# Performance work log

Hardware: AMD Instinct MI355X
Metric: run time of the kernel (lower is better)

The kernel has to match this reference:

```python
import jax, jax.numpy as jnp
import numpy as np

N_LORAS = 8   # number of adapters (experts)
RANK = 16     # rank per adapter; rmoe = N_LORAS * RANK = 128
TEMP = 1.0    # self.T


def setup_inputs() -> dict:
    key = jax.random.key(0)
    ks = jax.random.split(key, 7)
    B, S, D_IN, D_OUT = 4, 2048, 4096, 4096
    RMOE = N_LORAS * RANK
    x = jax.random.normal(ks[0], (B, S, D_IN), dtype=jnp.float32)
    base_w = jax.random.normal(ks[1], (D_OUT, D_IN), dtype=jnp.float32) / np.sqrt(D_IN)
    base_b = jax.random.normal(ks[2], (D_OUT,), dtype=jnp.float32) * 0.01
    # nn.init.normal_(lora_A.weight, std=1/r); lora_B zero-init in torch, use small random here
    lora_A = jax.random.normal(ks[3], (RMOE, D_IN), dtype=jnp.float32) / RANK
    lora_B = jax.random.normal(ks[4], (D_OUT, RMOE), dtype=jnp.float32) * 0.02
    router_w = jax.random.normal(ks[5], (N_LORAS, D_IN), dtype=jnp.float32) / np.sqrt(D_IN)
    # scaling[name] = lora_alpha / sqrt(r) per adapter (use_rslora)
    scalings = jnp.full((N_LORAS,), 32.0 / np.sqrt(RANK), dtype=jnp.float32)
    return {"x": x, "base_w": base_w, "base_b": base_b, "lora_A": lora_A,
            "lora_B": lora_B, "router_w": router_w, "scalings": scalings, "top_k": 2}


def reference(x, base_w, base_b, lora_A, lora_B, router_w, scalings, top_k):
    # Base dense layer: y = x W^T + b
    base_out = jnp.einsum('bsd,od->bso', x, base_w) + base_b

    # Router: per-token logits over adapters, top-k, softmax over selected
    logits = jnp.einsum('bsd,ed->bse', x, router_w) / TEMP          # [B,S,E]
    topv, topi = jax.lax.top_k(logits, top_k)                        # [B,S,K]
    gate_k = jax.nn.softmax(topv, axis=-1)                           # [B,S,K]
    # dense per-expert gate: scatter top-k weights back to E slots
    gate_e = jnp.sum(jax.nn.one_hot(topi, N_LORAS, dtype=gate_k.dtype)
                     * gate_k[..., None], axis=-2)                   # [B,S,E]

    # Fused LoRA: h = x A^T over the concatenated rank dim, mask ranks by gate*scaling
    h = jnp.einsum('bsd,rd->bsr', x, lora_A)                         # [B,S,RMOE]
    rank_w = jnp.repeat(gate_e * scalings, RANK, axis=-1)            # [B,S,RMOE]
    lora_out = jnp.einsum('bsr,or->bso', h * rank_w, lora_B)         # [B,S,O]

    return base_out + lora_out
```

## Files before the change

### kernel.cpp

```cpp
#include <hip/hip_runtime.h>
#include <cstdint>

typedef unsigned short u16;
typedef float  f32x4 __attribute__((ext_vector_type(4)));
typedef short  s16x4 __attribute__((ext_vector_type(4)));
typedef short  s16x8 __attribute__((ext_vector_type(8)));

#define D_IN  4096
#define D_OUT 4096
#define RMOE  128
#define KAUG  4224
#define NTOK  8192

__device__ __forceinline__ u16 f2bf(float f) {
    unsigned u = __builtin_bit_cast(unsigned, f);
    unsigned r = u + 0x7fffu + ((u >> 16) & 1u);
    return (u16)(r >> 16);
}

__device__ __forceinline__ void gload16(const void* g, void* l) {
    __builtin_amdgcn_global_load_lds(
        (const __attribute__((address_space(1))) void*)g,
        (__attribute__((address_space(3))) void*)l, 16, 0, 0);
}

__global__ __launch_bounds__(256)
void prep_kernel(const float* __restrict__ x, const float* __restrict__ rw,
                 const float* __restrict__ scal, const float* __restrict__ bw,
                 const float* __restrict__ lA, const float* __restrict__ lB,
                 u16* __restrict__ Xaug, u16* __restrict__ Waug,
                 u16* __restrict__ A16, float* __restrict__ gates) {
    if (blockIdx.x < 2048) {
        int wave = threadIdx.x >> 6, lane = threadIdx.x & 63;
        int t = blockIdx.x * 4 + wave;
        const float4* xp = (const float4*)(x + (long)t * D_IN);
        u16* xa = Xaug + (long)t * KAUG;
        float acc[8];
#pragma unroll
        for (int e = 0; e < 8; ++e) acc[e] = 0.f;
#pragma unroll 4
        for (int i = 0; i < 16; ++i) {
            float4 xv = xp[i * 64 + lane];
            s16x4 o;
            o[0] = (short)f2bf(xv.x); o[1] = (short)f2bf(xv.y);
            o[2] = (short)f2bf(xv.z); o[3] = (short)f2bf(xv.w);
            *(s16x4*)(xa + (i * 64 + lane) * 4) = o;
#pragma unroll
            for (int e = 0; e < 8; ++e) {
                float4 wv = ((const float4*)(rw + (long)e * D_IN))[i * 64 + lane];
                acc[e] += xv.x * wv.x + xv.y * wv.y + xv.z * wv.z + xv.w * wv.w;
            }
        }
#pragma unroll
        for (int e = 0; e < 8; ++e) {
#pragma unroll
            for (int off = 32; off > 0; off >>= 1)
                acc[e] += __shfl_xor(acc[e], off, 64);
        }
        if (lane == 0) {
            int i1 = 0; float v1 = acc[0];
#pragma unroll
            for (int e = 1; e < 8; ++e) if (acc[e] > v1) { v1 = acc[e]; i1 = e; }
            int i2 = -1; float v2 = -3.4e38f;
#pragma unroll
            for (int e = 0; e < 8; ++e) if (e != i1 && acc[e] > v2) { v2 = acc[e]; i2 = e; }
            float g1 = 1.f / (1.f + expf(v2 - v1));
            float g2 = 1.f - g1;
            float* gp = gates + (long)t * 8;
#pragma unroll
            for (int e = 0; e < 8; ++e)
                gp[e] = (e == i1) ? g1 * scal[e] : ((e == i2) ? g2 * scal[e] : 0.f);
        }
    } else {
        const long nw = (long)D_OUT * D_IN / 8;
        const long nb = (long)D_OUT * RMOE / 8;
        long tid = (long)(blockIdx.x - 2048) * 256 + threadIdx.x;
        const float* src; u16* dst;
        if (tid < nw) {
            long e = tid * 8; long row = e >> 12; long col = e & 4095;
            src = bw + e; dst = Waug + row * KAUG + col;
        } else if (tid < nw + nb) {
            long e = (tid - nw) * 8; long row = e >> 7; long col = e & 127;
            src = lB + e; dst = Waug + row * KAUG + D_IN + col;
        } else {
            long e = (tid - nw - nb) * 8;
            src = lA + e; dst = A16 + e;
        }
        float4 a = ((const float4*)src)[0];
        float4 b = ((const float4*)src)[1];
        s16x8 o;
        o[0] = (short)f2bf(a.x); o[1] = (short)f2bf(a.y);
        o[2] = (short)f2bf(a.z); o[3] = (short)f2bf(a.w);
        o[4] = (short)f2bf(b.x); o[5] = (short)f2bf(b.y);
        o[6] = (short)f2bf(b.z); o[7] = (short)f2bf(b.w);
        *(s16x8*)dst = o;
    }
}

__global__ __launch_bounds__(256)
void lora_h_kernel(u16* __restrict__ Xaug, const u16* __restrict__ A16,
                   const float* __restrict__ gates) {
    __shared__ u16 sX[64 * 32];
    __shared__ u16 sW[32 * 32];
    int tid = threadIdx.x, wave = tid >> 6, lane = tid & 63;
    int bm = blockIdx.x >> 2, bn = blockIdx.x & 3;
    long m0 = (long)bm * 64; int n0 = bn * 32;
    int wr = wave >> 1, wc = wave & 1;
    int rowA = tid >> 2, oct = tid & 3;
    const u16* gx = Xaug + (m0 + rowA) * KAUG + oct * 8;
    const u16* gw = A16 + (long)(n0 + rowA) * D_IN + oct * 8;
    u16* lx = sX + wave * 512;
    u16* lw = sW + wave * 512;
    int cl = lane & 15, kh = lane >> 4;
    int aoff[2];
#pragma unroll
    for (int i = 0; i < 2; ++i)
        aoff[i] = (wr * 32 + i * 16 + cl) * 32 + kh * 8;
    int boff = (wc * 16 + cl) * 32 + kh * 8;
    f32x4 acc2[2];
    acc2[0] = (f32x4){0.f, 0.f, 0.f, 0.f};
    acc2[1] = (f32x4){0.f, 0.f, 0.f, 0.f};
    for (int kt = 0; kt < 128; ++kt) {
        __syncthreads();
        gload16(gx, lx);
        if (tid < 128) gload16(gw, lw);
        gx += 32; gw += 32;
        __syncthreads();
        s16x8 a[2], b;
        a[0] = *(const s16x8*)&sX[aoff[0]];
        a[1] = *(const s16x8*)&sX[aoff[1]];
        b = *(const s16x8*)&sW[boff];
#pragma unroll
        for (int mi = 0; mi < 2; ++mi)
            acc2[mi] = __builtin_amdgcn_mfma_f32_16x16x32_bf16(
                a[mi], b, acc2[mi], 0, 0, 0);
    }
    int col = n0 + wc * 16 + cl;
    int g = col >> 4;
#pragma unroll
    for (int mi = 0; mi < 2; ++mi) {
#pragma unroll
        for (int r = 0; r < 4; ++r) {
            long tok = m0 + wr * 32 + mi * 16 + kh * 4 + r;
            float v = acc2[mi][r] * gates[tok * 8 + g];
            Xaug[tok * KAUG + D_IN + col] = f2bf(v);
        }
    }
}

__global__ __launch_bounds__(512, 4)
void main_gemm(const u16* __restrict__ Xaug, const u16* __restrict__ Waug,
               const float* __restrict__ bias, float* __restrict__ out) {
    __shared__ u16 lds[2 * 12288];
    const int tid = threadIdx.x;
    const int wave = tid >> 6, lane = tid & 63;
    const int cl = lane & 15, kh = lane >> 4;
    const int wr = wave >> 1, wc = wave & 1;

    int bid = blockIdx.x;
    int swz = (bid & 7) * 128 + (bid >> 3);
    long m0 = (long)(swz & 31) * 256;
    long n0 = (long)(swz >> 5) * 128;

    const int rA = tid >> 2;
    const int sl = (((tid & 3) ^ ((tid >> 3) & 3))) * 8;
    const u16* gA0 = Xaug + (m0 + rA) * KAUG + sl;
    const u16* gA1 = Xaug + (m0 + 128 + rA) * KAUG + sl;
    const u16* gB0 = Waug + (n0 + rA) * KAUG + sl;
    const int wbase = wave * 512;

    const int swk = (kh ^ ((cl >> 1) & 3)) * 8;
    const int aob = (wr * 64 + cl) * 32 + swk;
    const int bob = 8192 + (wc * 64 + cl) * 32 + swk;

    f32x4 acc[4][4];
#pragma unroll
    for (int m = 0; m < 4; ++m)
#pragma unroll
        for (int n = 0; n < 4; ++n) acc[m][n] = (f32x4){0.f, 0.f, 0.f, 0.f};

#define STAGE(t) do { u16* L = lds + ((t) & 1) * 12288 + wbase;              \
        gload16(gA0 + (t) * 32, L);                                          \
        gload16(gA1 + (t) * 32, L + 4096);                                   \
        gload16(gB0 + (t) * 32, L + 8192); } while (0)

    s16x8 av[4], bv[4];

    STAGE(0);

    for (int t = 0; t < 132; ++t) {
        asm volatile("s_waitcnt vmcnt(0)" ::: "memory");
        __builtin_amdgcn_s_barrier();
        __builtin_amdgcn_sched_barrier(0);
        if (t + 1 < 132) STAGE(t + 1);
        const u16* Lb = lds + (t & 1) * 12288;
#pragma unroll
        for (int m = 0; m < 4; ++m) av[m] = *(const s16x8*)&Lb[aob + m * 512];
#pragma unroll
        for (int n = 0; n < 4; ++n) bv[n] = *(const s16x8*)&Lb[bob + n * 512];
        asm volatile("s_waitcnt lgkmcnt(0)" ::: "memory");
        __builtin_amdgcn_sched_barrier(0);
        __builtin_amdgcn_s_setprio(1);
#pragma unroll
        for (int m = 0; m < 4; ++m)
#pragma unroll
            for (int n = 0; n < 4; ++n)
                acc[m][n] = __builtin_amdgcn_mfma_f32_16x16x32_bf16(
                    av[m], bv[n], acc[m][n], 0, 0, 0);
        __builtin_amdgcn_s_setprio(0);
    }
#undef STAGE

#pragma unroll
    for (int n = 0; n < 4; ++n) {
        long col = n0 + wc * 64 + n * 16 + cl;
        float bvv = bias[col];
#pragma unroll
        for (int m = 0; m < 4; ++m) {
            long row = m0 + wr * 64 + m * 16 + kh * 4;
#pragma unroll
            for (int r = 0; r < 4; ++r)
                out[(row + r) * (long)D_OUT + col] = acc[m][n][r] + bvv;
        }
    }
}

extern "C" void kernel_launch(void* const* d_in, const int* in_sizes, int n_in,
                              void* d_out, int out_size, void* d_ws, size_t ws_size,
                              hipStream_t stream) {
    const float* x  = (const float*)d_in[0];
    const float* bw = (const float*)d_in[1];
    const float* bb = (const float*)d_in[2];
    const float* lA = (const float*)d_in[3];
    const float* lB = (const float*)d_in[4];
    const float* rw = (const float*)d_in[5];
    const float* sc = (const float*)d_in[6];
    float* out = (float*)d_out;

    char* ws = (char*)d_ws;
    u16* Xaug  = (u16*)ws;
    u16* Waug  = (u16*)(ws + 69206016);
    u16* A16   = (u16*)(ws + 103809024);
    float* gates = (float*)(ws + 104857600);

    prep_kernel<<<10752, 256, 0, stream>>>(x, rw, sc, bw, lA, lB,
                                           Xaug, Waug, A16, gates);
    lora_h_kernel<<<512, 256, 0, stream>>>(Xaug, A16, gates);
    main_gemm<<<1024, 512, 0, stream>>>(Xaug, Waug, bb, out);
}
```

Baseline: 418.4 us.

## Enlarge main GEMM tile to 256x256 with K=64 stages and interleaved MFMA/loads

Grows the main GEMM block tile from 256x128 to 256x256, so each of the 8 waves now computes a 128x64 output patch. The K step per stage goes from 32 to 64 with an 8-way XOR swizzle, and the grid is halved. The main loop is restructured into quarter-steps that interleave LDS reads, MFMA groups and async global-to-LDS loads, with partial vmcnt waits so prefetch overlaps compute. This raises arithmetic intensity and cuts global traffic per FLOP. In exchange it uses more LDS (128KB) and registers, lowers occupancy to 2 blocks per CU, and adds many more barriers per K step.

After: 380.1 us. 1.1x faster.

```diff
diff --git a/kernel.cpp b/kernel.cpp
--- a/kernel.cpp
+++ b/kernel.cpp
@@ -148,76 +148,123 @@
     }
 }
 
-__global__ __launch_bounds__(512, 4)
+__global__ __launch_bounds__(512, 2)
 void main_gemm(const u16* __restrict__ Xaug, const u16* __restrict__ Waug,
                const float* __restrict__ bias, float* __restrict__ out) {
-    __shared__ u16 lds[2 * 12288];
+    __shared__ u16 lds[65536];
     const int tid = threadIdx.x;
     const int wave = tid >> 6, lane = tid & 63;
     const int cl = lane & 15, kh = lane >> 4;
-    const int wr = wave >> 1, wc = wave & 1;
+    const int wr = wave >> 2, wc = wave & 3;
 
     int bid = blockIdx.x;
-    int swz = (bid & 7) * 128 + (bid >> 3);
+    int swz = (bid & 7) * 64 + (bid >> 3);
     long m0 = (long)(swz & 31) * 256;
-    long n0 = (long)(swz >> 5) * 128;
-
-    const int rA = tid >> 2;
-    const int sl = (((tid & 3) ^ ((tid >> 3) & 3))) * 8;
-    const u16* gA0 = Xaug + (m0 + rA) * KAUG + sl;
-    const u16* gA1 = Xaug + (m0 + 128 + rA) * KAUG + sl;
-    const u16* gB0 = Waug + (n0 + rA) * KAUG + sl;
-    const int wbase = wave * 512;
-
-    const int swk = (kh ^ ((cl >> 1) & 3)) * 8;
-    const int aob = (wr * 64 + cl) * 32 + swk;
-    const int bob = 8192 + (wc * 64 + cl) * 32 + swk;
-
-    f32x4 acc[4][4];
-#pragma unroll
-    for (int m = 0; m < 4; ++m)
+    long n0 = (long)(swz >> 5) * 256;
+
+    const int rbase = tid >> 3;
+    const int sstg = ((tid & 7) ^ ((tid >> 3) & 7)) * 8;
+    const u16* gA = Xaug + (m0 + rbase) * KAUG + sstg;
+    const u16* gB = Waug + (n0 + rbase) * KAUG + sstg;
+    const int wst = (tid >> 6) * 512;
+
+    const int sk0 = ((kh) ^ (cl & 7)) * 8;
+    const int sk1 = ((4 + kh) ^ (cl & 7)) * 8;
+    const int ab0 = wr * 8192 + cl * 64;
+    const int bb0 = 32768 + wc * 4096 + cl * 64;
+
+    f32x4 acc[8][4];
+#pragma unroll
+    for (int m = 0; m < 8; ++m)
 #pragma unroll
         for (int n = 0; n < 4; ++n) acc[m][n] = (f32x4){0.f, 0.f, 0.f, 0.f};
 
-#define STAGE(t) do { u16* L = lds + ((t) & 1) * 12288 + wbase;              \
-        gload16(gA0 + (t) * 32, L);                                          \
-        gload16(gA1 + (t) * 32, L + 4096);                                   \
-        gload16(gB0 + (t) * 32, L + 8192); } while (0)
-
-    s16x8 av[4], bv[4];
-
-    STAGE(0);
-
-    for (int t = 0; t < 132; ++t) {
-        asm volatile("s_waitcnt vmcnt(0)" ::: "memory");
-        __builtin_amdgcn_s_barrier();
-        __builtin_amdgcn_sched_barrier(0);
-        if (t + 1 < 132) STAGE(t + 1);
-        const u16* Lb = lds + (t & 1) * 12288;
-#pragma unroll
-        for (int m = 0; m < 4; ++m) av[m] = *(const s16x8*)&Lb[aob + m * 512];
-#pragma unroll
-        for (int n = 0; n < 4; ++n) bv[n] = *(const s16x8*)&Lb[bob + n * 512];
-        asm volatile("s_waitcnt lgkmcnt(0)" ::: "memory");
-        __builtin_amdgcn_sched_barrier(0);
-        __builtin_amdgcn_s_setprio(1);
-#pragma unroll
-        for (int m = 0; m < 4; ++m)
-#pragma unroll
-            for (int n = 0; n < 4; ++n)
-                acc[m][n] = __builtin_amdgcn_mfma_f32_16x16x32_bf16(
-                    av[m], bv[n], acc[m][n], 0, 0, 0);
-        __builtin_amdgcn_s_setprio(0);
-    }
-#undef STAGE
+    s16x8 av[2][2], bv[4][2];
+
+#define STAGE_A(kt, ht) do {                                                 \
+        const u16* g_ = gA + ((long)(ht) * 128) * KAUG + (kt) * 64;          \
+        u16* d_ = lds + ((kt) & 1) * 16384 + (ht) * 8192 + wst;              \
+        gload16(g_, d_);                                                     \
+        gload16(g_ + (long)64 * KAUG, d_ + 4096); } while (0)
+#define STAGE_B(kt, ht) do {                                                 \
+        const u16* g_ = gB + ((long)(ht) * 128) * KAUG + (kt) * 64;          \
+        u16* d_ = lds + 32768 + ((kt) & 1) * 16384 + (ht) * 8192 + wst;      \
+        gload16(g_, d_);                                                     \
+        gload16(g_ + (long)64 * KAUG, d_ + 4096); } while (0)
+#define RD_B(BUFO) do {                                                      \
+        const u16* Lb_ = lds + (BUFO) + bb0;                                 \
+        _Pragma("unroll")                                                    \
+        for (int n_ = 0; n_ < 4; ++n_) {                                     \
+            bv[n_][0] = *(const s16x8*)&Lb_[n_ * 1024 + sk0];                \
+            bv[n_][1] = *(const s16x8*)&Lb_[n_ * 1024 + sk1]; } } while (0)
+#define RD_A2(Q, BUFO) do {                                                  \
+        const u16* La_ = lds + (BUFO) + ab0 + (Q) * 2048;                    \
+        av[0][0] = *(const s16x8*)&La_[sk0];                                 \
+        av[0][1] = *(const s16x8*)&La_[sk1];                                 \
+        av[1][0] = *(const s16x8*)&La_[1024 + sk0];                          \
+        av[1][1] = *(const s16x8*)&La_[1024 + sk1]; } while (0)
+#define MF(Q) do { __builtin_amdgcn_s_setprio(1);                            \
+        _Pragma("unroll")                                                    \
+        for (int j_ = 0; j_ < 2; ++j_)                                       \
+        _Pragma("unroll")                                                    \
+        for (int n_ = 0; n_ < 4; ++n_)                                       \
+        _Pragma("unroll")                                                    \
+        for (int kk_ = 0; kk_ < 2; ++kk_)                                    \
+            acc[2 * (Q) + j_][n_] = __builtin_amdgcn_mfma_f32_16x16x32_bf16( \
+                av[j_][kk_], bv[n_][kk_], acc[2 * (Q) + j_][n_], 0, 0, 0);   \
+        __builtin_amdgcn_s_setprio(0); } while (0)
+#define BAR1_LG() do { __builtin_amdgcn_s_barrier();                         \
+        asm volatile("s_waitcnt lgkmcnt(0)" ::: "memory");                   \
+        __builtin_amdgcn_sched_barrier(0); } while (0)
+#define BAR2() do { __builtin_amdgcn_s_barrier();                            \
+        __builtin_amdgcn_sched_barrier(0); } while (0)
+
+    STAGE_A(0, 0); STAGE_A(0, 1);
+    STAGE_B(0, 0); STAGE_B(0, 1);
+    STAGE_B(1, 0); STAGE_B(1, 1);
+    asm volatile("s_waitcnt vmcnt(4)" ::: "memory");
+    BAR2();
+
+    for (int i = 0; i < 33; ++i) {
+        const int k1 = 2 * i + 1, k2 = 2 * i + 2, k3 = 2 * i + 3;
+        const bool ok = (i < 32);
+        RD_B(0); RD_A2(0, 0); STAGE_A(k1, 0);
+        BAR1_LG(); MF(0); BAR2();
+        RD_A2(1, 0); STAGE_A(k1, 1);
+        BAR1_LG(); MF(1); BAR2();
+        RD_A2(2, 0); if (ok) STAGE_B(k2, 0);
+        BAR1_LG(); MF(2); BAR2();
+        RD_A2(3, 0); if (ok) STAGE_B(k2, 1);
+        BAR1_LG(); MF(3);
+        if (ok) asm volatile("s_waitcnt vmcnt(4)" ::: "memory");
+        else    asm volatile("s_waitcnt vmcnt(0)" ::: "memory");
+        BAR2();
+        RD_B(16384); RD_A2(0, 16384); if (ok) STAGE_A(k2, 0);
+        BAR1_LG(); MF(0); BAR2();
+        RD_A2(1, 16384); if (ok) STAGE_A(k2, 1);
+        BAR1_LG(); MF(1); BAR2();
+        RD_A2(2, 16384); if (ok) STAGE_B(k3, 0);
+        BAR1_LG(); MF(2); BAR2();
+        RD_A2(3, 16384); if (ok) STAGE_B(k3, 1);
+        BAR1_LG(); MF(3);
+        if (ok) asm volatile("s_waitcnt vmcnt(4)" ::: "memory");
+        BAR2();
+    }
+#undef STAGE_A
+#undef STAGE_B
+#undef RD_B
+#undef RD_A2
+#undef MF
+#undef BAR1_LG
+#undef BAR2
 
 #pragma unroll
     for (int n = 0; n < 4; ++n) {
         long col = n0 + wc * 64 + n * 16 + cl;
         float bvv = bias[col];
 #pragma unroll
-        for (int m = 0; m < 4; ++m) {
-            long row = m0 + wr * 64 + m * 16 + kh * 4;
+        for (int m = 0; m < 8; ++m) {
+            long row = m0 + wr * 128 + m * 16 + kh * 4;
 #pragma unroll
             for (int r = 0; r < 4; ++r)
                 out[(row + r) * (long)D_OUT + col] = acc[m][n][r] + bvv;
@@ -246,5 +293,5 @@
     prep_kernel<<<10752, 256, 0, stream>>>(x, rw, sc, bw, lA, lB,
                                            Xaug, Waug, A16, gates);
     lora_h_kernel<<<512, 256, 0, stream>>>(Xaug, A16, gates);
-    main_gemm<<<1024, 512, 0, stream>>>(Xaug, Waug, bb, out);
-}
+    main_gemm<<<512, 512, 0, stream>>>(Xaug, Waug, bb, out);
+}
```
